# Optimization experiments

Hardware: AMD Instinct MI355X
Metric: run time of the kernel (lower is better)

Reference implementation:

```python
import jax, jax.numpy as jnp
import numpy as np

S, B, D_MODEL, H = 2048, 2, 1024, 16
DH = D_MODEL // H
SCALE = 1.0 / np.sqrt(DH)
NEG_INF = jnp.float32(-1e30)


def setup_inputs() -> dict:
    key = jax.random.key(0)
    ks = jax.random.split(key, 12)
    std = 1.0 / np.sqrt(D_MODEL)
    inp = {
        "query": jax.random.normal(ks[0], (S, B, D_MODEL), jnp.float32),
        "key": jax.random.normal(ks[1], (S, B, D_MODEL), jnp.float32),
        "value": jax.random.normal(ks[2], (S, B, D_MODEL), jnp.float32),
        # causal mask, shape (seq_q, seq_k, 1) per prepare_mask asserts
        "mask": jnp.tril(jnp.ones((S, S), dtype=bool))[:, :, None],
        # params stored (in, out) for x @ W
        "Wq": jax.random.normal(ks[3], (D_MODEL, H * DH), jnp.float32) * std,
        "bq": jnp.zeros((H * DH,), jnp.float32),
        "Wk": jax.random.normal(ks[4], (D_MODEL, H * DH), jnp.float32) * std,
        "bk": jnp.zeros((H * DH,), jnp.float32),
        "Wv": jax.random.normal(ks[5], (D_MODEL, H * DH), jnp.float32) * std,
        "bv": jnp.zeros((H * DH,), jnp.float32),
        "Wo": jax.random.normal(ks[6], (D_MODEL, D_MODEL), jnp.float32) * std,
        "bo": jnp.zeros((D_MODEL,), jnp.float32),
    }
    return inp


def reference(query, key, value, mask, Wq, bq, Wk, bk, Wv, bv, Wo, bo):
    seq_len, batch, _ = query.shape
    # project and split heads: (S, B, H, DH)
    q = (query @ Wq + bq).reshape(seq_len, batch, H, DH)
    k = (key @ Wk + bk).reshape(key.shape[0], batch, H, DH)
    v = (value @ Wv + bv).reshape(value.shape[0], batch, H, DH)
    # scores: (seq_q, batch, heads, seq_k)
    scores = jnp.einsum("ibhd,jbhd->ibhj", q, k) * SCALE
    # mask (seq_q, seq_k, batch_or_1) -> broadcast to (seq_q, batch, 1, seq_k)
    m = jnp.transpose(mask, (0, 2, 1))[:, :, None, :]
    scores = jnp.where(m, scores, NEG_INF)
    attn = jax.nn.softmax(scores, axis=-1)  # dropout_prob=0.0 (eval)
    x = jnp.einsum("ibhj,jbhd->ibhd", attn, v)
    x = x.reshape(seq_len, batch, H * DH)
    return x @ Wo + bo
```

## Files before the change

kernel.cpp:

```cpp
#include <hip/hip_runtime.h>
#include <hip/hip_bf16.h>
#include <cstdint>

#define S_LEN 2048
#define BATCH 2
#define DM    1024
#define NH    16
#define DH    64
#define SL2E  0.18033688011112042f

typedef short s8v __attribute__((ext_vector_type(8)));
typedef float f4v __attribute__((ext_vector_type(4)));

__device__ __forceinline__ ushort f2bf(float x) {
  union { float f; uint32_t u; } v; v.f = x;
  uint32_t r = v.u + 0x7fffu + ((v.u >> 16) & 1u);
  return (ushort)(r >> 16);
}
__device__ __forceinline__ uint32_t fbits(float x) {
  union { float f; uint32_t u; } v; v.f = x; return v.u;
}
__device__ __forceinline__ uint32_t bfrnd(uint32_t u) {
  return u + 0x7fffu + ((u >> 16) & 1u);
}
__device__ __forceinline__ uint32_t packbf(uint32_t flo, uint32_t fhi) {
  return __builtin_amdgcn_perm(bfrnd(fhi), bfrnd(flo), 0x07060302u);
}

typedef __attribute__((address_space(1))) const void gas_void;
typedef __attribute__((address_space(3))) void las_void;
__device__ __forceinline__ void gld16(void* l, const void* g) {
  __builtin_amdgcn_global_load_lds((gas_void*)(uintptr_t)g,
                                   (las_void*)(uintptr_t)l, 16, 0, 0);
}

__global__ __launch_bounds__(256)
void prep(const float* W0, const float* W1, const float* W2, const float* W3,
          ushort* T0, ushort* T1, ushort* T2, ushort* T3,
          const float* X0, const float* X1, const float* X2,
          ushort* O0, ushort* O1, ushort* O2) {
  const int z = blockIdx.z;
  if (z < 4) {
    if (blockIdx.x >= 1024) return;
    const float* W = z == 0 ? W0 : z == 1 ? W1 : z == 2 ? W2 : W3;
    ushort*      T = z == 0 ? T0 : z == 1 ? T1 : z == 2 ? T2 : T3;
    __shared__ ushort tile[32][33];
    const int n0 = (blockIdx.x & 31) * 32, k0 = (blockIdx.x >> 5) * 32;
    const int tx = threadIdx.x & 31, ty = threadIdx.x >> 5;
    #pragma unroll
    for (int r = ty; r < 32; r += 8)
      tile[r][tx] = f2bf(W[(size_t)(k0 + r) * DM + n0 + tx]);
    __syncthreads();
    #pragma unroll
    for (int r = ty; r < 32; r += 8)
      T[(size_t)(n0 + r) * DM + k0 + tx] = tile[tx][r];
  } else {
    const float* X = z == 4 ? X0 : z == 5 ? X1 : X2;
    ushort*      O = z == 4 ? O0 : z == 5 ? O1 : O2;
    const size_t i = ((size_t)blockIdx.x * 256 + threadIdx.x) * 4;
    const float4 v = *(const float4*)(X + i);
    ushort4 h;
    h.x = f2bf(v.x); h.y = f2bf(v.y); h.z = f2bf(v.z); h.w = f2bf(v.w);
    *(ushort4*)(O + i) = h;
  }
}

__global__ __launch_bounds__(256)
void gemm_qkv(const ushort* __restrict__ Xq, const ushort* __restrict__ Xk,
              const ushort* __restrict__ Xv,
              const ushort* __restrict__ Wqt, const ushort* __restrict__ Wkt,
              const ushort* __restrict__ Wvt,
              const float* __restrict__ bq, const float* __restrict__ bk,
              const float* __restrict__ bv,
              ushort* __restrict__ Qh, ushort* __restrict__ Kh,
              ushort* __restrict__ Vt) {
  const int z = blockIdx.z;
  const ushort* A    = z == 0 ? Xq  : z == 1 ? Xk  : Xv;
  const ushort* Bt   = z == 0 ? Wqt : z == 1 ? Wkt : Wvt;
  const float*  bias = z == 0 ? bq  : z == 1 ? bk  : bv;

  __shared__ __align__(16) ushort lds[2][16384];

  const int tid = threadIdx.x, lane = tid & 63, w = tid >> 6;
  const int wr = w >> 1, wc = w & 1;
  const int lrow = lane & 15, quad = lane >> 4;
  const int m0 = blockIdx.x * 128, n0 = blockIdx.y * 128;

  const int srow = lane >> 3;
  const int scol = ((lane & 7) ^ srow) * 8;

  const ushort* gA[4]; const ushort* gB[4];
  int oA[4], oB[4];
  #pragma unroll
  for (int t = 0; t < 4; t++) {
    const int c = 4 * w + t;
    gA[t] = A  + (size_t)(m0 + c * 8 + srow) * DM + scol;
    oA[t] = c * 512;
    gB[t] = Bt + (size_t)(n0 + c * 8 + srow) * DM + scol;
    oB[t] = 8192 + c * 512;
  }

  const int f8 = lrow & 7;
  int pa[2][4], pb[2][4];
  #pragma unroll
  for (int kk = 0; kk < 2; kk++)
    #pragma unroll
    for (int i = 0; i < 4; i++) {
      pa[kk][i] = (wr * 64 + i * 16 + lrow) * 64 + (((kk * 4 + quad) ^ f8) * 8);
      pb[kk][i] = 8192 + (wc * 64 + i * 16 + lrow) * 64 + (((kk * 4 + quad) ^ f8) * 8);
    }

  f4v acc[4][4];
  #pragma unroll
  for (int i = 0; i < 4; i++)
    #pragma unroll
    for (int j = 0; j < 4; j++)
      acc[i][j] = f4v{0.f, 0.f, 0.f, 0.f};

  #pragma unroll
  for (int t = 0; t < 4; t++) {
    gld16(&lds[0][oA[t]], gA[t]);
    gld16(&lds[0][oB[t]], gB[t]);
  }

  for (int ks = 0; ks < 16; ks++) {
    __syncthreads();
    const ushort* buf = lds[ks & 1];
    if (ks < 15) {
      ushort* nb = lds[(ks + 1) & 1];
      const int ko = (ks + 1) * 64;
      #pragma unroll
      for (int t = 0; t < 4; t++) {
        gld16(nb + oA[t], gA[t] + ko);
        gld16(nb + oB[t], gB[t] + ko);
      }
    }
    #pragma unroll
    for (int kk = 0; kk < 2; kk++) {
      s8v af[4], bf[4];
      #pragma unroll
      for (int i = 0; i < 4; i++) af[i] = *(const s8v*)(buf + pa[kk][i]);
      #pragma unroll
      for (int j = 0; j < 4; j++) bf[j] = *(const s8v*)(buf + pb[kk][j]);
      #pragma unroll
      for (int i = 0; i < 4; i++)
        #pragma unroll
        for (int j = 0; j < 4; j++)
          acc[i][j] = __builtin_amdgcn_mfma_f32_16x16x32_bf16(af[i], bf[j], acc[i][j], 0, 0, 0);
    }
  }

  if (z <= 1) {
    ushort* O = (z == 0) ? Qh : Kh;
    #pragma unroll
    for (int i = 0; i < 4; i++)
      #pragma unroll
      for (int j = 0; j < 4; j++) {
        const int n = n0 + wc * 64 + j * 16 + lrow;
        const float bval = bias[n];
        const int mb = m0 + wr * 64 + i * 16 + quad * 4;
        #pragma unroll
        for (int r = 0; r < 4; r++) {
          const int m = mb + r;
          const int s = m >> 1, b = m & 1;
          const int h = n >> 6, d = n & 63;
          O[((size_t)(b * NH + h) * S_LEN + s) * DH + d] = f2bf(acc[i][j][r] + bval);
        }
      }
  } else {
    __syncthreads();
    ushort* tw = &lds[0][0] + w * 5120;
    #pragma unroll
    for (int i = 0; i < 4; i++)
      #pragma unroll
      for (int j = 0; j < 4; j++) {
        const int n_l = j * 16 + lrow;
        const float bval = bias[n0 + wc * 64 + n_l];
        const int sbase = i * 8 + quad * 2;
        const uint32_t p0 = packbf(fbits(acc[i][j][0] + bval), fbits(acc[i][j][2] + bval));
        const uint32_t p1 = packbf(fbits(acc[i][j][1] + bval), fbits(acc[i][j][3] + bval));
        *(uint32_t*)&tw[n_l * 40 + sbase]        = p0;
        *(uint32_t*)&tw[2560 + n_l * 40 + sbase] = p1;
      }
    const int s0 = (m0 >> 1) + wr * 32;
    #pragma unroll
    for (int b = 0; b < 2; b++)
      #pragma unroll
      for (int p = 0; p < 4; p++) {
        const int d_l = p * 16 + (lane >> 2);
        const int c   = lane & 3;
        const s8v v = *(const s8v*)&tw[b * 2560 + d_l * 40 + c * 8];
        const int n = n0 + wc * 64 + d_l;
        const int h = n >> 6, d = n & 63;
        *(s8v*)&Vt[((size_t)(b * NH + h) * DH + d) * S_LEN + s0 + c * 8] = v;
      }
  }
}

__global__ __launch_bounds__(256)
void attn(const ushort* __restrict__ Qh, const ushort* __restrict__ Kh,
          const ushort* __restrict__ Vt, ushort* __restrict__ X,
          float* __restrict__ Opart, float* __restrict__ lpart) {
  __shared__ __align__(16) ushort Klds[2 * 64 * 64];
  __shared__ __align__(16) ushort Vlds[2 * 64 * 64];
  __shared__ __align__(16) ushort Plds[4][32 * 72];

  const int tid = threadIdx.x, lane = tid & 63, w = tid >> 6;
  const int lrow = lane & 15, quad = lane >> 4;
  const int bh = blockIdx.x;
  const int slot = blockIdx.y;
  int qt, jlo, jhi, part;
  if (slot < 8) { qt = slot; jlo = 0; jhi = 2 * qt + 2; part = -1; }
  else {
    const int s2 = slot - 8;
    qt = 8 + (s2 >> 1);
    const int half = s2 & 1;
    jlo = half * (qt + 1);
    jhi = jlo + (qt + 1);
    part = s2;
  }
  const int iw = qt * 128 + w * 32;

  const int srow = lane >> 3;
  const int scol = ((lane & 7) ^ srow) * 8;
  const ushort* gK0 = Kh + ((size_t)bh * S_LEN + 2 * w * 8 + srow) * DH + scol;
  const ushort* gK1 = gK0 + 8 * DH;
  const ushort* gV0 = Vt + ((size_t)bh * DH + 2 * w * 8 + srow) * S_LEN + scol;
  const ushort* gV1 = gV0 + 8 * S_LEN;
  ushort* lK0 = &Klds[2 * w * 512]; ushort* lK1 = lK0 + 512;
  ushort* lV0 = &Vlds[2 * w * 512]; ushort* lV1 = lV0 + 512;

  s8v aq[2][2];
  #pragma unroll
  for (int is = 0; is < 2; is++)
    #pragma unroll
    for (int kk = 0; kk < 2; kk++)
      aq[is][kk] = *(const s8v*)(Qh + ((size_t)bh * S_LEN + iw + is * 16 + lrow) * DH +
                                 kk * 32 + quad * 8);

  const int f8 = lrow & 7;
  const ushort* pk[4][2]; const ushort* pv[4][2];
  #pragma unroll
  for (int s4 = 0; s4 < 4; s4++)
    #pragma unroll
    for (int kk = 0; kk < 2; kk++) {
      pk[s4][kk] = &Klds[(s4 * 16 + lrow) * 64 + (((kk * 4 + quad) ^ f8) * 8)];
      pv[s4][kk] = &Vlds[(s4 * 16 + lrow) * 64 + (((kk * 4 + quad) ^ f8) * 8)];
    }
  ushort* pwr = &Plds[w][lrow * 72];

  f4v o[2][4];
  float ls[2] = {0.f, 0.f};
  #pragma unroll
  for (int is = 0; is < 2; is++)
    #pragma unroll
    for (int d4 = 0; d4 < 4; d4++) o[is][d4] = f4v{0.f, 0.f, 0.f, 0.f};

  {
    const int b0 = (jlo & 1) * 4096;
    const size_t j0 = (size_t)jlo * 64;
    gld16(lK0 + b0, gK0 + j0 * DH);
    gld16(lK1 + b0, gK1 + j0 * DH);
    gld16(lV0 + b0, gV0 + j0);
    gld16(lV1 + b0, gV1 + j0);
  }

  for (int jt = jlo; jt < jhi; jt++) {
    const int j0 = jt * 64;
    __syncthreads();
    const int cur = (jt & 1) * 4096;
    if (jt + 1 < jhi) {
      const int nxt = ((jt + 1) & 1) * 4096;
      const size_t jn = (size_t)(jt + 1) * 64;
      gld16(lK0 + nxt, gK0 + jn * DH);
      gld16(lK1 + nxt, gK1 + jn * DH);
      gld16(lV0 + nxt, gV0 + jn);
      gld16(lV1 + nxt, gV1 + jn);
    }
    if (j0 > iw + 31) continue;

    f4v sc[2][4];
    #pragma unroll
    for (int is = 0; is < 2; is++)
      #pragma unroll
      for (int s4 = 0; s4 < 4; s4++) sc[is][s4] = f4v{0.f, 0.f, 0.f, 0.f};
    #pragma unroll
    for (int s4 = 0; s4 < 4; s4++) {
      const s8v k0f = *(const s8v*)(pk[s4][0] + cur);
      const s8v k1f = *(const s8v*)(pk[s4][1] + cur);
      sc[0][s4] = __builtin_amdgcn_mfma_f32_16x16x32_bf16(k0f, aq[0][0], sc[0][s4], 0, 0, 0);
      sc[1][s4] = __builtin_amdgcn_mfma_f32_16x16x32_bf16(k0f, aq[1][0], sc[1][s4], 0, 0, 0);
      sc[0][s4] = __builtin_amdgcn_mfma_f32_16x16x32_bf16(k1f, aq[0][1], sc[0][s4], 0, 0, 0);
      sc[1][s4] = __builtin_amdgcn_mfma_f32_16x16x32_bf16(k1f, aq[1][1], sc[1][s4], 0, 0, 0);
    }

    const bool needmask = (j0 + 63) > iw;
    #pragma unroll
    for (int is = 0; is < 2; is++) {
      const int ig = iw + is * 16 + lrow;
      #pragma unroll
      for (int s4 = 0; s4 < 4; s4++) {
        float e0 = exp2f(sc[is][s4][0] * SL2E);
        float e1 = exp2f(sc[is][s4][1] * SL2E);
        float e2 = exp2f(sc[is][s4][2] * SL2E);
        float e3 = exp2f(sc[is][s4][3] * SL2E);
        if (needmask) {
          const int jb = j0 + s4 * 16 + quad * 4;
          e0 = (jb + 0 > ig) ? 0.f : e0;
          e1 = (jb + 1 > ig) ? 0.f : e1;
          e2 = (jb + 2 > ig) ? 0.f : e2;
          e3 = (jb + 3 > ig) ? 0.f : e3;
        }
        ls[is] += (e0 + e1) + (e2 + e3);
        uint2 pk2;
        pk2.x = packbf(fbits(e0), fbits(e1));
        pk2.y = packbf(fbits(e2), fbits(e3));
        *(uint2*)&pwr[is * 16 * 72 + s4 * 16 + quad * 4] = pk2;
      }
    }

    s8v ap[2][2];
    #pragma unroll
    for (int is = 0; is < 2; is++)
      #pragma unroll
      for (int kt = 0; kt < 2; kt++)
        ap[is][kt] = *(const s8v*)&pwr[is * 16 * 72 + kt * 32 + quad * 8];
    #pragma unroll
    for (int d4 = 0; d4 < 4; d4++) {
      const s8v v0 = *(const s8v*)(pv[d4][0] + cur);
      const s8v v1 = *(const s8v*)(pv[d4][1] + cur);
      o[0][d4] = __builtin_amdgcn_mfma_f32_16x16x32_bf16(ap[0][0], v0, o[0][d4], 0, 0, 0);
      o[1][d4] = __builtin_amdgcn_mfma_f32_16x16x32_bf16(ap[1][0], v0, o[1][d4], 0, 0, 0);
      o[0][d4] = __builtin_amdgcn_mfma_f32_16x16x32_bf16(ap[0][1], v1, o[0][d4], 0, 0, 0);
      o[1][d4] = __builtin_amdgcn_mfma_f32_16x16x32_bf16(ap[1][1], v1, o[1][d4], 0, 0, 0);
    }
  }

  #pragma unroll
  for (int is = 0; is < 2; is++) {
    ls[is] += __shfl_xor(ls[is], 16, 64);
    ls[is] += __shfl_xor(ls[is], 32, 64);
  }

  if (part < 0) {
    const int bb = bh >> 4, h = bh & 15;
    #pragma unroll
    for (int is = 0; is < 2; is++)
      #pragma unroll
      for (int r = 0; r < 4; r++) {
        const float lv = __shfl(ls[is], quad * 16 + quad * 4 + r, 64);
        const float inv = 1.0f / lv;
        const int sg = iw + is * 16 + quad * 4 + r;
        #pragma unroll
        for (int d4 = 0; d4 < 4; d4++)
          X[((size_t)sg * BATCH + bb) * DM + h * DH + d4 * 16 + lrow] =
              f2bf(o[is][d4][r] * inv);
      }
  } else {
    float* Op = Opart + ((size_t)(bh * 16 + part)) * 8192 + (size_t)w * 2048;
    #pragma unroll
    for (int is = 0; is < 2; is++)
      #pragma unroll
      for (int r = 0; r < 4; r++) {
        const int row_l = is * 16 + quad * 4 + r;
        #pragma unroll
        for (int d4 = 0; d4 < 4; d4++)
          Op[row_l * 64 + d4 * 16 + lrow] = o[is][d4][r];
      }
    if (quad == 0) {
      float* lp = lpart + (size_t)(bh * 16 + part) * 128 + w * 32;
      lp[lrow]      = ls[0];
      lp[16 + lrow] = ls[1];
    }
  }
}

__global__ __launch_bounds__(256)
void combine(const float* __restrict__ Opart, const float* __restrict__ lpart,
             ushort* __restrict__ X) {
  const size_t gid = (size_t)blockIdx.x * 256 + threadIdx.x;
  const int dv  = gid & 15;
  const int row = (gid >> 4) & 127;
  const int bh  = (gid >> 11) & 31;
  const int qt8 = gid >> 16;
  const int pa = qt8 * 2, pb = pa + 1;
  const size_t ba = ((size_t)(bh * 16 + pa)) * 8192 + row * 64 + dv * 4;
  const size_t bb_ = ((size_t)(bh * 16 + pb)) * 8192 + row * 64 + dv * 4;
  const float4 va = *(const float4*)(Opart + ba);
  const float4 vb = *(const float4*)(Opart + bb_);
  const float l = lpart[(size_t)(bh * 16 + pa) * 128 + row] +
                  lpart[(size_t)(bh * 16 + pb) * 128 + row];
  const float inv = 1.0f / l;
  const int qpos = (qt8 + 8) * 128 + row;
  const int b = bh >> 4, h = bh & 15;
  ushort4 hv;
  hv.x = f2bf((va.x + vb.x) * inv);
  hv.y = f2bf((va.y + vb.y) * inv);
  hv.z = f2bf((va.z + vb.z) * inv);
  hv.w = f2bf((va.w + vb.w) * inv);
  *(ushort4*)&X[(((size_t)qpos * BATCH + b) * NH + h) * DH + dv * 4] = hv;
}

__global__ __launch_bounds__(256)
void gemm_out(const ushort* __restrict__ A, const ushort* __restrict__ Bt,
              const float* __restrict__ bias, float* __restrict__ C) {
  __shared__ __align__(16) ushort lds[2][16384];

  const int tid = threadIdx.x, lane = tid & 63, w = tid >> 6;
  const int wr = w >> 1, wc = w & 1;
  const int lrow = lane & 15, quad = lane >> 4;
  const int m0 = blockIdx.x * 128, n0 = blockIdx.y * 128;

  const int srow = lane >> 3;
  const int scol = ((lane & 7) ^ srow) * 8;

  const ushort* gA[4]; const ushort* gB[4];
  int oA[4], oB[4];
  #pragma unroll
  for (int t = 0; t < 4; t++) {
    const int c = 4 * w + t;
    gA[t] = A  + (size_t)(m0 + c * 8 + srow) * DM + scol;
    oA[t] = c * 512;
    gB[t] = Bt + (size_t)(n0 + c * 8 + srow) * DM + scol;
    oB[t] = 8192 + c * 512;
  }

  const int f8 = lrow & 7;
  int pa[2][4], pb[2][4];
  #pragma unroll
  for (int kk = 0; kk < 2; kk++)
    #pragma unroll
    for (int i = 0; i < 4; i++) {
      pa[kk][i] = (wr * 64 + i * 16 + lrow) * 64 + (((kk * 4 + quad) ^ f8) * 8);
      pb[kk][i] = 8192 + (wc * 64 + i * 16 + lrow) * 64 + (((kk * 4 + quad) ^ f8) * 8);
    }

  f4v acc[4][4];
  #pragma unroll
  for (int i = 0; i < 4; i++)
    #pragma unroll
    for (int j = 0; j < 4; j++)
      acc[i][j] = f4v{0.f, 0.f, 0.f, 0.f};

  #pragma unroll
  for (int t = 0; t < 4; t++) {
    gld16(&lds[0][oA[t]], gA[t]);
    gld16(&lds[0][oB[t]], gB[t]);
  }

  for (int ks = 0; ks < 16; ks++) {
    __syncthreads();
    const ushort* buf = lds[ks & 1];
    if (ks < 15) {
      ushort* nb = lds[(ks + 1) & 1];
      const int ko = (ks + 1) * 64;
      #pragma unroll
      for (int t = 0; t < 4; t++) {
        gld16(nb + oA[t], gA[t] + ko);
        gld16(nb + oB[t], gB[t] + ko);
      }
    }
    #pragma unroll
    for (int kk = 0; kk < 2; kk++) {
      s8v af[4], bf[4];
      #pragma unroll
      for (int i = 0; i < 4; i++) af[i] = *(const s8v*)(buf + pa[kk][i]);
      #pragma unroll
      for (int j = 0; j < 4; j++) bf[j] = *(const s8v*)(buf + pb[kk][j]);
      #pragma unroll
      for (int i = 0; i < 4; i++)
        #pragma unroll
        for (int j = 0; j < 4; j++)
          acc[i][j] = __builtin_amdgcn_mfma_f32_16x16x32_bf16(af[i], bf[j], acc[i][j], 0, 0, 0);
    }
  }

  #pragma unroll
  for (int i = 0; i < 4; i++)
    #pragma unroll
    for (int j = 0; j < 4; j++) {
      const int n = n0 + wc * 64 + j * 16 + lrow;
      const float bval = bias[n];
      const int mb = m0 + wr * 64 + i * 16 + quad * 4;
      #pragma unroll
      for (int r = 0; r < 4; r++)
        C[(size_t)(mb + r) * DM + n] = acc[i][j][r] + bval;
    }
}

extern "C" void kernel_launch(void* const* d_in, const int* in_sizes, int n_in,
                              void* d_out, int out_size, void* d_ws, size_t ws_size,
                              hipStream_t stream) {
  const float* query = (const float*)d_in[0];
  const float* key_  = (const float*)d_in[1];
  const float* value = (const float*)d_in[2];
  const float* Wq = (const float*)d_in[4];
  const float* bq = (const float*)d_in[5];
  const float* Wk = (const float*)d_in[6];
  const float* bk = (const float*)d_in[7];
  const float* Wv = (const float*)d_in[8];
  const float* bv = (const float*)d_in[9];
  const float* Wo = (const float*)d_in[10];
  const float* bo = (const float*)d_in[11];

  ushort* Wqt = (ushort*)d_ws;
  ushort* Wkt = Wqt + (size_t)1024 * 1024;
  ushort* Wvt = Wkt + (size_t)1024 * 1024;
  ushort* Wot = Wvt + (size_t)1024 * 1024;
  ushort* Xbq = Wot + (size_t)1024 * 1024;
  ushort* Xbk = Xbq + (size_t)4 * 1024 * 1024;
  ushort* Xbv = Xbk + (size_t)4 * 1024 * 1024;
  ushort* Qh  = Xbv + (size_t)4 * 1024 * 1024;
  ushort* Kh  = Qh  + (size_t)4 * 1024 * 1024;
  ushort* Vt  = Kh  + (size_t)4 * 1024 * 1024;
  float*  Opart = (float*)Xbk;
  float*  lpart = (float*)(Vt + (size_t)4 * 1024 * 1024);
  ushort* Xa  = Xbq;

  prep<<<dim3(4096, 1, 7), 256, 0, stream>>>(Wq, Wk, Wv, Wo, Wqt, Wkt, Wvt, Wot,
                                             query, key_, value, Xbq, Xbk, Xbv);
  gemm_qkv<<<dim3(32, 8, 3), 256, 0, stream>>>(Xbq, Xbk, Xbv,
                                               Wqt, Wkt, Wvt, bq, bk, bv,
                                               Qh, Kh, Vt);
  attn<<<dim3(32, 24), 256, 0, stream>>>(Qh, Kh, Vt, Xa, Opart, lpart);
  combine<<<2048, 256, 0, stream>>>(Opart, lpart, Xa);
  gemm_out<<<dim3(32, 8), 256, 0, stream>>>(Xa, Wot, bo, (float*)d_out);
}
```

Baseline: 241.3 us.

## Rebalance attention split-K partitions, shrink GEMM K-tile, store partials in bf16

New measurement: 234.4 us. 1.03x faster.

```diff
diff --git a/kernel.cpp b/kernel.cpp
--- a/kernel.cpp
+++ b/kernel.cpp
@@ -7,7 +7,6 @@
 #define DM    1024
 #define NH    16
 #define DH    64
-#define SL2E  0.18033688011112042f
 
 typedef short s8v __attribute__((ext_vector_type(8)));
 typedef float f4v __attribute__((ext_vector_type(4)));
@@ -17,6 +16,9 @@
   uint32_t r = v.u + 0x7fffu + ((v.u >> 16) & 1u);
   return (ushort)(r >> 16);
 }
+__device__ __forceinline__ float bf2f(ushort u) {
+  union { uint32_t u; float f; } v; v.u = (uint32_t)u << 16; return v.f;
+}
 __device__ __forceinline__ uint32_t fbits(float x) {
   union { float f; uint32_t u; } v; v.f = x; return v.u;
 }
@@ -25,6 +27,9 @@
 }
 __device__ __forceinline__ uint32_t packbf(uint32_t flo, uint32_t fhi) {
   return __builtin_amdgcn_perm(bfrnd(fhi), bfrnd(flo), 0x07060302u);
+}
+__device__ __forceinline__ uint32_t packbf_tr(float lo, float hi) {
+  return __builtin_amdgcn_perm(fbits(hi), fbits(lo), 0x07060302u);
 }
 
 typedef __attribute__((address_space(1))) const void gas_void;
@@ -79,36 +84,33 @@
   const ushort* Bt   = z == 0 ? Wqt : z == 1 ? Wkt : Wvt;
   const float*  bias = z == 0 ? bq  : z == 1 ? bk  : bv;
 
-  __shared__ __align__(16) ushort lds[2][16384];
+  __shared__ __align__(16) ushort lds[20480];
 
   const int tid = threadIdx.x, lane = tid & 63, w = tid >> 6;
   const int wr = w >> 1, wc = w & 1;
   const int lrow = lane & 15, quad = lane >> 4;
   const int m0 = blockIdx.x * 128, n0 = blockIdx.y * 128;
 
-  const int srow = lane >> 3;
-  const int scol = ((lane & 7) ^ srow) * 8;
-
-  const ushort* gA[4]; const ushort* gB[4];
-  int oA[4], oB[4];
-  #pragma unroll
-  for (int t = 0; t < 4; t++) {
-    const int c = 4 * w + t;
-    gA[t] = A  + (size_t)(m0 + c * 8 + srow) * DM + scol;
+  const int sr4 = lane >> 2;
+  const int scol = ((lane & 3) ^ (sr4 & 3)) * 8;
+
+  const ushort* gA[2]; const ushort* gB[2];
+  int oA[2], oB[2];
+  #pragma unroll
+  for (int t = 0; t < 2; t++) {
+    const int c = 2 * w + t;
+    gA[t] = A  + (size_t)(m0 + c * 16 + sr4) * DM + scol;
     oA[t] = c * 512;
-    gB[t] = Bt + (size_t)(n0 + c * 8 + srow) * DM + scol;
-    oB[t] = 8192 + c * 512;
-  }
-
-  const int f8 = lrow & 7;
-  int pa[2][4], pb[2][4];
-  #pragma unroll
-  for (int kk = 0; kk < 2; kk++)
-    #pragma unroll
-    for (int i = 0; i < 4; i++) {
-      pa[kk][i] = (wr * 64 + i * 16 + lrow) * 64 + (((kk * 4 + quad) ^ f8) * 8);
-      pb[kk][i] = 8192 + (wc * 64 + i * 16 + lrow) * 64 + (((kk * 4 + quad) ^ f8) * 8);
-    }
+    gB[t] = Bt + (size_t)(n0 + c * 16 + sr4) * DM + scol;
+    oB[t] = 4096 + c * 512;
+  }
+
+  int pa[4], pb[4];
+  #pragma unroll
+  for (int i = 0; i < 4; i++) {
+    pa[i] = (wr * 64 + i * 16 + lrow) * 32 + ((quad ^ (lrow & 3)) * 8);
+    pb[i] = 4096 + (wc * 64 + i * 16 + lrow) * 32 + ((quad ^ (lrow & 3)) * 8);
+  }
 
   f4v acc[4][4];
   #pragma unroll
@@ -118,36 +120,33 @@
       acc[i][j] = f4v{0.f, 0.f, 0.f, 0.f};
 
   #pragma unroll
-  for (int t = 0; t < 4; t++) {
-    gld16(&lds[0][oA[t]], gA[t]);
-    gld16(&lds[0][oB[t]], gB[t]);
-  }
-
-  for (int ks = 0; ks < 16; ks++) {
+  for (int t = 0; t < 2; t++) {
+    gld16(&lds[oA[t]], gA[t]);
+    gld16(&lds[oB[t]], gB[t]);
+  }
+
+  for (int ks = 0; ks < 32; ks++) {
     __syncthreads();
-    const ushort* buf = lds[ks & 1];
-    if (ks < 15) {
-      ushort* nb = lds[(ks + 1) & 1];
-      const int ko = (ks + 1) * 64;
-      #pragma unroll
-      for (int t = 0; t < 4; t++) {
-        gld16(nb + oA[t], gA[t] + ko);
-        gld16(nb + oB[t], gB[t] + ko);
-      }
-    }
-    #pragma unroll
-    for (int kk = 0; kk < 2; kk++) {
-      s8v af[4], bf[4];
-      #pragma unroll
-      for (int i = 0; i < 4; i++) af[i] = *(const s8v*)(buf + pa[kk][i]);
-      #pragma unroll
-      for (int j = 0; j < 4; j++) bf[j] = *(const s8v*)(buf + pb[kk][j]);
-      #pragma unroll
-      for (int i = 0; i < 4; i++)
-        #pragma unroll
-        for (int j = 0; j < 4; j++)
-          acc[i][j] = __builtin_amdgcn_mfma_f32_16x16x32_bf16(af[i], bf[j], acc[i][j], 0, 0, 0);
-    }
+    const int bo = (ks & 1) * 8192;
+    if (ks < 31) {
+      const int nb = ((ks + 1) & 1) * 8192;
+      const int ko = (ks + 1) * 32;
+      #pragma unroll
+      for (int t = 0; t < 2; t++) {
+        gld16(&lds[nb + oA[t]], gA[t] + ko);
+        gld16(&lds[nb + oB[t]], gB[t] + ko);
+      }
+    }
+    s8v af[4], bf[4];
+    #pragma unroll
+    for (int i = 0; i < 4; i++) af[i] = *(const s8v*)&lds[bo + pa[i]];
+    #pragma unroll
+    for (int j = 0; j < 4; j++) bf[j] = *(const s8v*)&lds[bo + pb[j]];
+    #pragma unroll
+    for (int i = 0; i < 4; i++)
+      #pragma unroll
+      for (int j = 0; j < 4; j++)
+        acc[i][j] = __builtin_amdgcn_mfma_f32_16x16x32_bf16(af[i], bf[j], acc[i][j], 0, 0, 0);
   }
 
   if (z <= 1) {
@@ -169,7 +168,7 @@
       }
   } else {
     __syncthreads();
-    ushort* tw = &lds[0][0] + w * 5120;
+    ushort* tw = lds + w * 5120;
     #pragma unroll
     for (int i = 0; i < 4; i++)
       #pragma unroll
@@ -200,7 +199,7 @@
 __global__ __launch_bounds__(256)
 void attn(const ushort* __restrict__ Qh, const ushort* __restrict__ Kh,
           const ushort* __restrict__ Vt, ushort* __restrict__ X,
-          float* __restrict__ Opart, float* __restrict__ lpart) {
+          ushort* __restrict__ Opart, float* __restrict__ lpart) {
   __shared__ __align__(16) ushort Klds[2 * 64 * 64];
   __shared__ __align__(16) ushort Vlds[2 * 64 * 64];
   __shared__ __align__(16) ushort Plds[4][32 * 72];
@@ -209,17 +208,14 @@
   const int lrow = lane & 15, quad = lane >> 4;
   const int bh = blockIdx.x;
   const int slot = blockIdx.y;
-  int qt, jlo, jhi, part;
-  if (slot < 8) { qt = slot; jlo = 0; jhi = 2 * qt + 2; part = -1; }
-  else {
-    const int s2 = slot - 8;
-    qt = 8 + (s2 >> 1);
-    const int half = s2 & 1;
-    jlo = half * (qt + 1);
-    jhi = jlo + (qt + 1);
-    part = s2;
-  }
-  const int iw = qt * 128 + w * 32;
+  int qt, part, nparts;
+  if (slot < 18)      { qt = 15 - slot / 3;        part = slot % 3;        nparts = 3; }
+  else if (slot < 30) { qt = 9  - (slot - 18) / 2; part = (slot - 18) % 2; nparts = 2; }
+  else                { qt = 33 - slot;            part = 0;               nparts = 1; }
+  const int nj  = 2 * qt + 2;
+  const int jlo = part * nj / nparts;
+  const int jhi = (part + 1) * nj / nparts;
+  const int iw  = qt * 128 + w * 32;
 
   const int srow = lane >> 3;
   const int scol = ((lane & 7) ^ srow) * 8;
@@ -300,10 +296,10 @@
       const int ig = iw + is * 16 + lrow;
       #pragma unroll
       for (int s4 = 0; s4 < 4; s4++) {
-        float e0 = exp2f(sc[is][s4][0] * SL2E);
-        float e1 = exp2f(sc[is][s4][1] * SL2E);
-        float e2 = exp2f(sc[is][s4][2] * SL2E);
-        float e3 = exp2f(sc[is][s4][3] * SL2E);
+        float e0 = __expf(sc[is][s4][0] * 0.125f);
+        float e1 = __expf(sc[is][s4][1] * 0.125f);
+        float e2 = __expf(sc[is][s4][2] * 0.125f);
+        float e3 = __expf(sc[is][s4][3] * 0.125f);
         if (needmask) {
           const int jb = j0 + s4 * 16 + quad * 4;
           e0 = (jb + 0 > ig) ? 0.f : e0;
@@ -313,8 +309,8 @@
         }
         ls[is] += (e0 + e1) + (e2 + e3);
         uint2 pk2;
-        pk2.x = packbf(fbits(e0), fbits(e1));
-        pk2.y = packbf(fbits(e2), fbits(e3));
+        pk2.x = packbf_tr(e0, e1);
+        pk2.y = packbf_tr(e2, e3);
         *(uint2*)&pwr[is * 16 * 72 + s4 * 16 + quad * 4] = pk2;
       }
     }
@@ -342,7 +338,7 @@
     ls[is] += __shfl_xor(ls[is], 32, 64);
   }
 
-  if (part < 0) {
+  if (nparts == 1) {
     const int bb = bh >> 4, h = bh & 15;
     #pragma unroll
     for (int is = 0; is < 2; is++)
@@ -357,7 +353,7 @@
               f2bf(o[is][d4][r] * inv);
       }
   } else {
-    float* Op = Opart + ((size_t)(bh * 16 + part)) * 8192 + (size_t)w * 2048;
+    ushort* Op = Opart + ((size_t)(bh * 30 + slot) * 128 + w * 32) * 64;
     #pragma unroll
     for (int is = 0; is < 2; is++)
       #pragma unroll
@@ -365,10 +361,10 @@
         const int row_l = is * 16 + quad * 4 + r;
         #pragma unroll
         for (int d4 = 0; d4 < 4; d4++)
-          Op[row_l * 64 + d4 * 16 + lrow] = o[is][d4][r];
+          Op[row_l * 64 + d4 * 16 + lrow] = f2bf(o[is][d4][r]);
       }
     if (quad == 0) {
-      float* lp = lpart + (size_t)(bh * 16 + part) * 128 + w * 32;
+      float* lp = lpart + (size_t)(bh * 30 + slot) * 128 + w * 32;
       lp[lrow]      = ls[0];
       lp[16 + lrow] = ls[1];
     }
@@ -376,64 +372,70 @@
 }
 
 __global__ __launch_bounds__(256)
-void combine(const float* __restrict__ Opart, const float* __restrict__ lpart,
+void combine(const ushort* __restrict__ Opart, const float* __restrict__ lpart,
              ushort* __restrict__ X) {
-  const size_t gid = (size_t)blockIdx.x * 256 + threadIdx.x;
-  const int dv  = gid & 15;
-  const int row = (gid >> 4) & 127;
-  const int bh  = (gid >> 11) & 31;
-  const int qt8 = gid >> 16;
-  const int pa = qt8 * 2, pb = pa + 1;
-  const size_t ba = ((size_t)(bh * 16 + pa)) * 8192 + row * 64 + dv * 4;
-  const size_t bb_ = ((size_t)(bh * 16 + pb)) * 8192 + row * 64 + dv * 4;
-  const float4 va = *(const float4*)(Opart + ba);
-  const float4 vb = *(const float4*)(Opart + bb_);
-  const float l = lpart[(size_t)(bh * 16 + pa) * 128 + row] +
-                  lpart[(size_t)(bh * 16 + pb) * 128 + row];
+  const uint32_t gid = blockIdx.x * 256 + threadIdx.x;
+  const int dv   = gid & 15;
+  const int row  = (gid >> 4) & 127;
+  const int rest = gid >> 11;
+  const int qi   = rest % 12;
+  const int bh   = rest / 12;
+  const int qt   = 4 + qi;
+  int s0, c;
+  if (qt >= 10) { s0 = 3 * (15 - qt); c = 3; }
+  else          { s0 = 18 + 2 * (9 - qt); c = 2; }
+
+  float a0 = 0.f, a1 = 0.f, a2 = 0.f, a3 = 0.f, l = 0.f;
+  #pragma unroll
+  for (int p = 0; p < 3; p++) {
+    if (p < c) {
+      const size_t base = ((size_t)(bh * 30 + s0 + p) * 128 + row);
+      const ushort4 v = *(const ushort4*)&Opart[base * 64 + dv * 4];
+      a0 += bf2f(v.x); a1 += bf2f(v.y); a2 += bf2f(v.z); a3 += bf2f(v.w);
+      l += lpart[base];
+    }
+  }
   const float inv = 1.0f / l;
-  const int qpos = (qt8 + 8) * 128 + row;
+  const int qpos = qt * 128 + row;
   const int b = bh >> 4, h = bh & 15;
   ushort4 hv;
-  hv.x = f2bf((va.x + vb.x) * inv);
-  hv.y = f2bf((va.y + vb.y) * inv);
-  hv.z = f2bf((va.z + vb.z) * inv);
-  hv.w = f2bf((va.w + vb.w) * inv);
+  hv.x = f2bf(a0 * inv);
+  hv.y = f2bf(a1 * inv);
+  hv.z = f2bf(a2 * inv);
+  hv.w = f2bf(a3 * inv);
   *(ushort4*)&X[(((size_t)qpos * BATCH + b) * NH + h) * DH + dv * 4] = hv;
 }
 
 __global__ __launch_bounds__(256)
 void gemm_out(const ushort* __restrict__ A, const ushort* __restrict__ Bt,
               const float* __restrict__ bias, float* __restrict__ C) {
-  __shared__ __align__(16) ushort lds[2][16384];
+  __shared__ __align__(16) ushort lds[16384];
 
   const int tid = threadIdx.x, lane = tid & 63, w = tid >> 6;
   const int wr = w >> 1, wc = w & 1;
   const int lrow = lane & 15, quad = lane >> 4;
   const int m0 = blockIdx.x * 128, n0 = blockIdx.y * 128;
 
-  const int srow = lane >> 3;
-  const int scol = ((lane & 7) ^ srow) * 8;
-
-  const ushort* gA[4]; const ushort* gB[4];
-  int oA[4], oB[4];
-  #pragma unroll
-  for (int t = 0; t < 4; t++) {
-    const int c = 4 * w + t;
-    gA[t] = A  + (size_t)(m0 + c * 8 + srow) * DM + scol;
+  const int sr4 = lane >> 2;
+  const int scol = ((lane & 3) ^ (sr4 & 3)) * 8;
+
+  const ushort* gA[2]; const ushort* gB[2];
+  int oA[2], oB[2];
+  #pragma unroll
+  for (int t = 0; t < 2; t++) {
+    const int c = 2 * w + t;
+    gA[t] = A  + (size_t)(m0 + c * 16 + sr4) * DM + scol;
     oA[t] = c * 512;
-    gB[t] = Bt + (size_t)(n0 + c * 8 + srow) * DM + scol;
-    oB[t] = 8192 + c * 512;
-  }
-
-  const int f8 = lrow & 7;
-  int pa[2][4], pb[2][4];
-  #pragma unroll
-  for (int kk = 0; kk < 2; kk++)
-    #pragma unroll
-    for (int i = 0; i < 4; i++) {
-      pa[kk][i] = (wr * 64 + i * 16 + lrow) * 64 + (((kk * 4 + quad) ^ f8) * 8);
-      pb[kk][i] = 8192 + (wc * 64 + i * 16 + lrow) * 64 + (((kk * 4 + quad) ^ f8) * 8);
-    }
+    gB[t] = Bt + (size_t)(n0 + c * 16 + sr4) * DM + scol;
+    oB[t] = 4096 + c * 512;
+  }
+
+  int pa[4], pb[4];
+  #pragma unroll
+  for (int i = 0; i < 4; i++) {
+    pa[i] = (wr * 64 + i * 16 + lrow) * 32 + ((quad ^ (lrow & 3)) * 8);
+    pb[i] = 4096 + (wc * 64 + i * 16 + lrow) * 32 + ((quad ^ (lrow & 3)) * 8);
+  }
 
   f4v acc[4][4];
   #pragma unroll
@@ -443,36 +445,33 @@
       acc[i][j] = f4v{0.f, 0.f, 0.f, 0.f};
 
   #pragma unroll
-  for (int t = 0; t < 4; t++) {
-    gld16(&lds[0][oA[t]], gA[t]);
-    gld16(&lds[0][oB[t]], gB[t]);
-  }
-
-  for (int ks = 0; ks < 16; ks++) {
+  for (int t = 0; t < 2; t++) {
+    gld16(&lds[oA[t]], gA[t]);
+    gld16(&lds[oB[t]], gB[t]);
+  }
+
+  for (int ks = 0; ks < 32; ks++) {
     __syncthreads();
-    const ushort* buf = lds[ks & 1];
-    if (ks < 15) {
-      ushort* nb = lds[(ks + 1) & 1];
-      const int ko = (ks + 1) * 64;
-      #pragma unroll
-      for (int t = 0; t < 4; t++) {
-        gld16(nb + oA[t], gA[t] + ko);
-        gld16(nb + oB[t], gB[t] + ko);
-      }
-    }
-    #pragma unroll
-    for (int kk = 0; kk < 2; kk++) {
-      s8v af[4], bf[4];
-      #pragma unroll
-      for (int i = 0; i < 4; i++) af[i] = *(const s8v*)(buf + pa[kk][i]);
-      #pragma unroll
-      for (int j = 0; j < 4; j++) bf[j] = *(const s8v*)(buf + pb[kk][j]);
-      #pragma unroll
-      for (int i = 0; i < 4; i++)
-        #pragma unroll
-        for (int j = 0; j < 4; j++)
-          acc[i][j] = __builtin_amdgcn_mfma_f32_16x16x32_bf16(af[i], bf[j], acc[i][j], 0, 0, 0);
-    }
+    const int bo = (ks & 1) * 8192;
+    if (ks < 31) {
+      const int nb = ((ks + 1) & 1) * 8192;
+      const int ko = (ks + 1) * 32;
+      #pragma unroll
+      for (int t = 0; t < 2; t++) {
+        gld16(&lds[nb + oA[t]], gA[t] + ko);
+        gld16(&lds[nb + oB[t]], gB[t] + ko);
+      }
+    }
+    s8v af[4], bf[4];
+    #pragma unroll
+    for (int i = 0; i < 4; i++) af[i] = *(const s8v*)&lds[bo + pa[i]];
+    #pragma unroll
+    for (int j = 0; j < 4; j++) bf[j] = *(const s8v*)&lds[bo + pb[j]];
+    #pragma unroll
+    for (int i = 0; i < 4; i++)
+      #pragma unroll
+      for (int j = 0; j < 4; j++)
+        acc[i][j] = __builtin_amdgcn_mfma_f32_16x16x32_bf16(af[i], bf[j], acc[i][j], 0, 0, 0);
   }
 
   #pragma unroll
@@ -513,8 +512,8 @@
   ushort* Qh  = Xbv + (size_t)4 * 1024 * 1024;
   ushort* Kh  = Qh  + (size_t)4 * 1024 * 1024;
   ushort* Vt  = Kh  + (size_t)4 * 1024 * 1024;
-  float*  Opart = (float*)Xbk;
-  float*  lpart = (float*)(Vt + (size_t)4 * 1024 * 1024);
+  ushort* Opart = Xbk;
+  float*  lpart = (float*)Wqt;
   ushort* Xa  = Xbq;
 
   prep<<<dim3(4096, 1, 7), 256, 0, stream>>>(Wq, Wk, Wv, Wo, Wqt, Wkt, Wvt, Wot,
@@ -522,7 +521,7 @@
   gemm_qkv<<<dim3(32, 8, 3), 256, 0, stream>>>(Xbq, Xbk, Xbv,
                                                Wqt, Wkt, Wvt, bq, bk, bv,
                                                Qh, Kh, Vt);
-  attn<<<dim3(32, 24), 256, 0, stream>>>(Qh, Kh, Vt, Xa, Opart, lpart);
-  combine<<<2048, 256, 0, stream>>>(Opart, lpart, Xa);
+  attn<<<dim3(32, 34), 256, 0, stream>>>(Qh, Kh, Vt, Xa, Opart, lpart);
+  combine<<<3072, 256, 0, stream>>>(Opart, lpart, Xa);
   gemm_out<<<dim3(32, 8), 256, 0, stream>>>(Xa, Wot, bo, (float*)d_out);
 }
```
